# Kernel optimization log

Hardware: AMD Instinct MI355X
Metric: run time of the kernel (lower is better)

Reference implementation:

```python
import jax, jax.numpy as jnp
import numpy as np

EMBED_DIM = 512  # channels C
B, H, W = 2, 64, 64


def _conv1x1(x, w, b):
    # x: [B, C, H, W]; w: [C_out, C_in]; b: [C_out]  (1x1 conv == per-pixel linear)
    return jnp.einsum('bchw,dc->bdhw', x, w) + b[None, :, None, None]


def setup_inputs() -> dict:
    key = jax.random.key(0)
    ks = jax.random.split(key, 9)
    C = EMBED_DIM
    s = 1.0 / np.sqrt(C)
    x = jax.random.normal(ks[0], (B, C, H, W), dtype=jnp.float32)
    wq = jax.random.normal(ks[1], (C, C), dtype=jnp.float32) * s
    bq = jax.random.normal(ks[2], (C,), dtype=jnp.float32) * 0.01
    wk = jax.random.normal(ks[3], (C, C), dtype=jnp.float32) * s
    bk = jax.random.normal(ks[4], (C,), dtype=jnp.float32) * 0.01
    wv = jax.random.normal(ks[5], (C, C), dtype=jnp.float32) * s
    bv = jax.random.normal(ks[6], (C,), dtype=jnp.float32) * 0.01
    wo = jax.random.normal(ks[7], (C, C), dtype=jnp.float32) * s
    bo = jax.random.normal(ks[8], (C,), dtype=jnp.float32) * 0.01
    return {"x": x, "wq": wq, "bq": bq, "wk": wk, "bk": bk,
            "wv": wv, "bv": bv, "wo": wo, "bo": bo}


def reference(x, wq, bq, wk, bk, wv, bv, wo, bo):
    b, c, h, w = x.shape
    n = h * w
    q = _conv1x1(x, wq, bq).reshape(b, c, n)
    k = _conv1x1(x, wk, bk).reshape(b, c, n)
    v = _conv1x1(x, wv, bv).reshape(b, c, n)
    # scores = q^T @ k over channel dim -> [b, n, n]; scale by sqrt(C) (scale=True)
    scores = jnp.einsum('bcn,bcm->bnm', q, k) / jnp.sqrt(jnp.asarray(c, x.dtype))
    attn = jax.nn.softmax(scores, axis=-1)
    # output = v @ attn^T -> [b, c, n]
    out = jnp.einsum('bcm,bnm->bcn', v, attn).reshape(b, c, h, w)
    return _conv1x1(out, wo, bo)
```

## Files before the change

### kernel.cpp

```cpp
#include <hip/hip_runtime.h>
#include <stdint.h>

typedef short s16x8 __attribute__((ext_vector_type(8)));
typedef unsigned short u16x8 __attribute__((ext_vector_type(8)));
typedef float f32x4 __attribute__((ext_vector_type(4)));

__device__ __forceinline__ float bf2f(unsigned short u) {
  union { unsigned u; float f; } c; c.u = ((unsigned)u) << 16; return c.f;
}
__device__ __forceinline__ unsigned short f2bf(float f) {
  union { float f; unsigned u; } c; c.f = f;
  unsigned u = c.u + 0x7fffu + ((c.u >> 16) & 1u);
  return (unsigned short)(u >> 16);
}

__device__ __forceinline__ void g2l16(const void* g, void* l) {
  __builtin_amdgcn_global_load_lds(
      (const __attribute__((address_space(1))) void*)(unsigned long long)g,
      (__attribute__((address_space(3))) void*)(unsigned)(unsigned long long)l,
      16, 0, 0);
}

template <int MODE, typename OutT>
__global__ __launch_bounds__(256) void gemm_abt(
    const unsigned short* __restrict__ A, int lda,
    const unsigned short* __restrict__ Bt, int ldb,
    OutT* __restrict__ C, int ldc,
    const float* __restrict__ bias,
    float* __restrict__ rowsum,
    int M, int N, int K, int nsplit,
    long long sA, long long sBt, long long sC, long long sSplit,
    float scale)
{
  __shared__ __align__(16) unsigned short smem[128 * 136];
  unsigned short* As = smem;
  unsigned short* Bs = smem + 128 * 64;

  const int ks = blockIdx.z % nsplit;
  const int bz = blockIdx.z / nsplit;
  A  += (long long)bz * sA;
  Bt += (long long)bz * sBt;
  C  += (long long)bz * sC + (long long)ks * sSplit;

  const int tile_m = blockIdx.y * 128;
  const int tile_n = blockIdx.x * 128;

  const int tid  = threadIdx.x;
  const int wid  = tid >> 6;
  const int lane = tid & 63;
  const int wm = (wid >> 1) * 64;
  const int wn = (wid & 1) * 64;
  const int lr = lane & 15;
  const int lq = lane >> 4;

  const int srow = lane >> 3;
  const int scol = ((lane & 7) ^ (srow & 7)) * 8;

  f32x4 acc[4][4];
  const f32x4 zero4 = {0.f, 0.f, 0.f, 0.f};
  #pragma unroll
  for (int i = 0; i < 4; ++i)
    #pragma unroll
    for (int j = 0; j < 4; ++j) acc[i][j] = zero4;

  const unsigned short* Arow = A  + (long long)tile_m * lda;
  const unsigned short* Brow = Bt + (long long)tile_n * ldb;

  const int kLen = K / nsplit;
  const int kBeg = ks * kLen;

  for (int k0 = kBeg; k0 < kBeg + kLen; k0 += 64) {
    #pragma unroll
    for (int c = 0; c < 4; ++c) {
      const int chunk = wid * 4 + c;
      const int row = chunk * 8 + srow;
      g2l16(Arow + (long long)row * lda + k0 + scol, As + chunk * 512);
      g2l16(Brow + (long long)row * ldb + k0 + scol, Bs + chunk * 512);
    }
    __syncthreads();
    #pragma unroll
    for (int kss = 0; kss < 2; ++kss) {
      const int cch = kss * 4 + lq;
      s16x8 af[4], bfr[4];
      #pragma unroll
      for (int i = 0; i < 4; ++i) {
        const int row = wm + i * 16 + lr;
        af[i] = *(const s16x8*)&As[row * 64 + ((cch ^ (row & 7)) * 8)];
      }
      #pragma unroll
      for (int j = 0; j < 4; ++j) {
        const int row = wn + j * 16 + lr;
        bfr[j] = *(const s16x8*)&Bs[row * 64 + ((cch ^ (row & 7)) * 8)];
      }
      #pragma unroll
      for (int i = 0; i < 4; ++i)
        #pragma unroll
        for (int j = 0; j < 4; ++j)
          acc[i][j] = __builtin_amdgcn_mfma_f32_16x16x32_bf16(af[i], bfr[j], acc[i][j], 0, 0, 0);
    }
    __syncthreads();
  }

  if constexpr (MODE == 3) {
    #pragma unroll
    for (int i = 0; i < 4; ++i) {
      const int row0 = tile_m + wm + i * 16 + lq * 4;
      #pragma unroll
      for (int j = 0; j < 4; ++j) {
        const int col = tile_n + wn + j * 16 + lr;
        const float inv = 1.0f / rowsum[(long long)bz * N + col];
        #pragma unroll
        for (int r = 0; r < 4; ++r) {
          float v = acc[i][j][r] * inv;
          if (ks == 0) v += bias[row0 + r];
          atomicAdd((float*)&C[(long long)(row0 + r) * ldc + col], v);
        }
      }
    }
  } else {
    #pragma unroll
    for (int i = 0; i < 4; ++i) {
      const int lrow0 = wm + i * 16 + lq * 4;
      float rsum[4] = {0.f, 0.f, 0.f, 0.f};
      #pragma unroll
      for (int j = 0; j < 4; ++j) {
        const int lcol = wn + j * 16 + lr;
        float bcol = 0.f;
        if (MODE == 1 && bias) bcol = bias[tile_n + lcol];
        #pragma unroll
        for (int r = 0; r < 4; ++r) {
          float v = acc[i][j][r] * scale + bcol;
          if (MODE == 2) { v = __expf(v); rsum[r] += v; }
          smem[(lrow0 + r) * 136 + lcol] = f2bf(v);
        }
      }
      if (MODE == 2) {
        #pragma unroll
        for (int r = 0; r < 4; ++r) {
          float s = rsum[r];
          s += __shfl_xor(s, 1); s += __shfl_xor(s, 2);
          s += __shfl_xor(s, 4); s += __shfl_xor(s, 8);
          if (lr == 0)
            atomicAdd(&rowsum[(long long)bz * M + tile_m + lrow0 + r], s);
        }
      }
    }
    __syncthreads();
    const int row = tid >> 1;
    const int cb = (tid & 1) * 64;
    unsigned short* Cg = (unsigned short*)C;
    #pragma unroll
    for (int k = 0; k < 8; ++k) {
      u16x8 v = *(const u16x8*)&smem[row * 136 + cb + k * 8];
      *(u16x8*)&Cg[(long long)(tile_m + row) * ldc + tile_n + cb + k * 8] = v;
    }
  }
}

__global__ __launch_bounds__(256) void cvt_weights(
    const float* __restrict__ wq, const float* __restrict__ wk,
    const float* __restrict__ wv, const float* __restrict__ wo,
    const float* __restrict__ bq, const float* __restrict__ bk,
    unsigned short* __restrict__ wqk_b, unsigned short* __restrict__ wvT_b,
    unsigned short* __restrict__ wo_b, float* __restrict__ bqk,
    float* __restrict__ rowsum, int n)
{
  const int i = blockIdx.x * 256 + threadIdx.x;
  if (i < n) {
    wqk_b[i]     = f2bf(wq[i]);
    wqk_b[n + i] = f2bf(wk[i]);
    wvT_b[i]     = f2bf(wv[(i & 511) * 512 + (i >> 9)]);
    wo_b[i]      = f2bf(wo[i]);
  }
  if (i < 512) {
    bqk[i]       = bq[i];
    bqk[512 + i] = bk[i];
  }
  if (i < 8192) rowsum[i] = 0.f;
}

__global__ __launch_bounds__(256) void bias_pp(
    const float* __restrict__ wo, const float* __restrict__ bv,
    const float* __restrict__ bo, float* __restrict__ bpp)
{
  const int w = threadIdx.x >> 6, lane = threadIdx.x & 63;
  const int d = blockIdx.x * 4 + w;
  const float* row = wo + (long long)d * 512;
  float s = 0.f;
  #pragma unroll
  for (int c = 0; c < 512; c += 64) s += row[c + lane] * bv[c + lane];
  #pragma unroll
  for (int o = 32; o > 0; o >>= 1) s += __shfl_xor(s, o, 64);
  if (lane == 0) bpp[d] = s + bo[d];
}

__global__ __launch_bounds__(256) void transpose_cn(
    const float* __restrict__ x, unsigned short* __restrict__ xT,
    int C, int N)
{
  __shared__ float tile[32][33];
  const long long boff = (long long)blockIdx.z * C * N;
  const int n0 = blockIdx.x * 32;
  const int c0 = blockIdx.y * 32;
  const int tx = threadIdx.x;
  const int ty = threadIdx.y;
  #pragma unroll
  for (int k = 0; k < 32; k += 8)
    tile[ty + k][tx] = x[boff + (long long)(c0 + ty + k) * N + n0 + tx];
  __syncthreads();
  #pragma unroll
  for (int k = 0; k < 32; k += 8)
    xT[boff + (long long)(n0 + ty + k) * C + c0 + tx] = f2bf(tile[tx][ty + k]);
}

extern "C" void kernel_launch(void* const* d_in, const int* in_sizes, int n_in,
                              void* d_out, int out_size, void* d_ws, size_t ws_size,
                              hipStream_t stream) {
  (void)in_sizes; (void)n_in; (void)ws_size;
  const float* x  = (const float*)d_in[0];
  const float* wq = (const float*)d_in[1];
  const float* bq = (const float*)d_in[2];
  const float* wk = (const float*)d_in[3];
  const float* bk = (const float*)d_in[4];
  const float* wv = (const float*)d_in[5];
  const float* bv = (const float*)d_in[6];
  const float* wo = (const float*)d_in[7];
  const float* bo = (const float*)d_in[8];
  float* out = (float*)d_out;

  const int Cc = 512, N = 4096, Bn = 2;
  const int CC = Cc * Cc;
  const long long NC  = (long long)N * Cc;
  const long long NC2 = (long long)N * 1024;
  const long long NN  = (long long)N * N;

  char* wsb = (char*)d_ws;
  unsigned short* wqk_b = (unsigned short*)wsb;
  unsigned short* wvT_b = wqk_b + 2LL * CC;
  unsigned short* wo_b  = wvT_b + CC;
  unsigned short* Wp    = wo_b + CC;
  float*          bqk   = (float*)(Wp + CC);
  float*          bpp   = bqk + 1024;
  float*          rsum  = bpp + 512;
  unsigned short* xT    = (unsigned short*)(rsum + 8192);
  unsigned short* qkT   = xT + Bn * NC;
  unsigned short* vo    = qkT + Bn * NC2;
  unsigned short* S     = vo + Bn * NC;

  const float inv_sqrt_c = 0.044194173824159216f;

  cvt_weights<<<dim3((CC + 255) / 256), 256, 0, stream>>>(
      wq, wk, wv, wo, bq, bk, wqk_b, wvT_b, wo_b, bqk, rsum, CC);
  bias_pp<<<dim3(128), 256, 0, stream>>>(wo, bv, bo, bpp);
  gemm_abt<1, unsigned short><<<dim3(4, 4, 1), 256, 0, stream>>>(
      wo_b, 512, wvT_b, 512, Wp, 512, nullptr, nullptr,
      512, 512, 512, 1, 0, 0, 0, 0, 1.0f);
  transpose_cn<<<dim3(N / 32, Cc / 32, Bn), dim3(32, 8), 0, stream>>>(x, xT, Cc, N);

  gemm_abt<1, unsigned short><<<dim3(8, N / 128, Bn), 256, 0, stream>>>(
      xT, Cc, wqk_b, Cc, qkT, 1024, bqk, nullptr, N, 1024, Cc, 1,
      NC, 0, NC2, 0, 1.0f);
  gemm_abt<2, unsigned short><<<dim3(N / 128, N / 128, Bn), 256, 0, stream>>>(
      qkT, 1024, qkT + 512, 1024, S, N, nullptr, rsum, N, N, Cc, 1,
      NC2, NC2, NN, 0, inv_sqrt_c);
  gemm_abt<1, unsigned short><<<dim3(N / 128, 4, Bn), 256, 0, stream>>>(
      Wp, 512, xT, 512, vo, N, nullptr, nullptr, 512, N, Cc, 1,
      0, NC, NC, 0, 1.0f);
  hipMemsetAsync(out, 0, (size_t)out_size * sizeof(float), stream);
  gemm_abt<3, float><<<dim3(N / 128, 4, Bn * 2), 256, 0, stream>>>(
      vo, N, S, N, out, N, bpp, rsum, 512, N, N, 2,
      NC, NN, NC, 0, 1.0f);
}
```

Measured before the change: 285.2 us.

## Fuse V projection into QK GEMM and replace atomic split-K with partial reduce

The folded Wo·Wv weight becomes a third block of a concatenated 1536-column weight, so x is projected to Q, K and the projected V in one GEMM. A bf16 transpose then lays out the V part for the final GEMM. The final attention-times-V GEMM now uses a 4-way K split that writes bf16 partial tiles through the normal epilogue, instead of a 2-way split doing fp32 atomicAdds into a zeroed output. A new elementwise kernel sums the four partials, applies the softmax row normalisation and adds the bias. This removes atomic contention and the memset and doubles block-level parallelism, at the cost of extra partial-buffer traffic, one more launch and extra bf16 rounding of partial sums.

```diff
diff --git a/kernel.cpp b/kernel.cpp
--- a/kernel.cpp
+++ b/kernel.cpp
@@ -21,11 +21,11 @@
       16, 0, 0);
 }
 
-template <int MODE, typename OutT>
+template <int MODE>
 __global__ __launch_bounds__(256) void gemm_abt(
     const unsigned short* __restrict__ A, int lda,
     const unsigned short* __restrict__ Bt, int ldb,
-    OutT* __restrict__ C, int ldc,
+    unsigned short* __restrict__ C, int ldc,
     const float* __restrict__ bias,
     float* __restrict__ rowsum,
     int M, int N, int K, int nsplit,
@@ -101,59 +101,40 @@
     __syncthreads();
   }
 
-  if constexpr (MODE == 3) {
+  #pragma unroll
+  for (int i = 0; i < 4; ++i) {
+    const int lrow0 = wm + i * 16 + lq * 4;
+    float rsum[4] = {0.f, 0.f, 0.f, 0.f};
     #pragma unroll
-    for (int i = 0; i < 4; ++i) {
-      const int row0 = tile_m + wm + i * 16 + lq * 4;
-      #pragma unroll
-      for (int j = 0; j < 4; ++j) {
-        const int col = tile_n + wn + j * 16 + lr;
-        const float inv = 1.0f / rowsum[(long long)bz * N + col];
-        #pragma unroll
-        for (int r = 0; r < 4; ++r) {
-          float v = acc[i][j][r] * inv;
-          if (ks == 0) v += bias[row0 + r];
-          atomicAdd((float*)&C[(long long)(row0 + r) * ldc + col], v);
-        }
+    for (int j = 0; j < 4; ++j) {
+      const int lcol = wn + j * 16 + lr;
+      float bcol = 0.f;
+      if (MODE == 1 && bias) bcol = bias[tile_n + lcol];
+      #pragma unroll
+      for (int r = 0; r < 4; ++r) {
+        float v = acc[i][j][r] * scale + bcol;
+        if (MODE == 2) { v = __expf(v); rsum[r] += v; }
+        smem[(lrow0 + r) * 136 + lcol] = f2bf(v);
       }
     }
-  } else {
-    #pragma unroll
-    for (int i = 0; i < 4; ++i) {
-      const int lrow0 = wm + i * 16 + lq * 4;
-      float rsum[4] = {0.f, 0.f, 0.f, 0.f};
-      #pragma unroll
-      for (int j = 0; j < 4; ++j) {
-        const int lcol = wn + j * 16 + lr;
-        float bcol = 0.f;
-        if (MODE == 1 && bias) bcol = bias[tile_n + lcol];
-        #pragma unroll
-        for (int r = 0; r < 4; ++r) {
-          float v = acc[i][j][r] * scale + bcol;
-          if (MODE == 2) { v = __expf(v); rsum[r] += v; }
-          smem[(lrow0 + r) * 136 + lcol] = f2bf(v);
-        }
-      }
-      if (MODE == 2) {
-        #pragma unroll
-        for (int r = 0; r < 4; ++r) {
-          float s = rsum[r];
-          s += __shfl_xor(s, 1); s += __shfl_xor(s, 2);
-          s += __shfl_xor(s, 4); s += __shfl_xor(s, 8);
-          if (lr == 0)
-            atomicAdd(&rowsum[(long long)bz * M + tile_m + lrow0 + r], s);
-        }
+    if (MODE == 2) {
+      #pragma unroll
+      for (int r = 0; r < 4; ++r) {
+        float s = rsum[r];
+        s += __shfl_xor(s, 1); s += __shfl_xor(s, 2);
+        s += __shfl_xor(s, 4); s += __shfl_xor(s, 8);
+        if (lr == 0)
+          atomicAdd(&rowsum[(long long)bz * M + tile_m + lrow0 + r], s);
       }
     }
-    __syncthreads();
-    const int row = tid >> 1;
-    const int cb = (tid & 1) * 64;
-    unsigned short* Cg = (unsigned short*)C;
-    #pragma unroll
-    for (int k = 0; k < 8; ++k) {
-      u16x8 v = *(const u16x8*)&smem[row * 136 + cb + k * 8];
-      *(u16x8*)&Cg[(long long)(tile_m + row) * ldc + tile_n + cb + k * 8] = v;
-    }
+  }
+  __syncthreads();
+  const int row = tid >> 1;
+  const int cb = (tid & 1) * 64;
+  #pragma unroll
+  for (int k = 0; k < 8; ++k) {
+    u16x8 v = *(const u16x8*)&smem[row * 136 + cb + k * 8];
+    *(u16x8*)&C[(long long)(tile_m + row) * ldc + tile_n + cb + k * 8] = v;
   }
 }
 
@@ -161,20 +142,21 @@
     const float* __restrict__ wq, const float* __restrict__ wk,
     const float* __restrict__ wv, const float* __restrict__ wo,
     const float* __restrict__ bq, const float* __restrict__ bk,
-    unsigned short* __restrict__ wqk_b, unsigned short* __restrict__ wvT_b,
-    unsigned short* __restrict__ wo_b, float* __restrict__ bqk,
+    unsigned short* __restrict__ W3, unsigned short* __restrict__ wvT_b,
+    unsigned short* __restrict__ wo_b, float* __restrict__ bqk3,
     float* __restrict__ rowsum, int n)
 {
   const int i = blockIdx.x * 256 + threadIdx.x;
   if (i < n) {
-    wqk_b[i]     = f2bf(wq[i]);
-    wqk_b[n + i] = f2bf(wk[i]);
-    wvT_b[i]     = f2bf(wv[(i & 511) * 512 + (i >> 9)]);
-    wo_b[i]      = f2bf(wo[i]);
+    W3[i]      = f2bf(wq[i]);
+    W3[n + i]  = f2bf(wk[i]);
+    wvT_b[i]   = f2bf(wv[(i & 511) * 512 + (i >> 9)]);
+    wo_b[i]    = f2bf(wo[i]);
   }
   if (i < 512) {
-    bqk[i]       = bq[i];
-    bqk[512 + i] = bk[i];
+    bqk3[i]        = bq[i];
+    bqk3[512 + i]  = bk[i];
+    bqk3[1024 + i] = 0.f;
   }
   if (i < 8192) rowsum[i] = 0.f;
 }
@@ -213,10 +195,56 @@
     xT[boff + (long long)(n0 + ty + k) * C + c0 + tx] = f2bf(tile[tx][ty + k]);
 }
 
+__global__ __launch_bounds__(256) void transpose_bf(
+    const unsigned short* __restrict__ src, int srcLd, long long sSrc,
+    unsigned short* __restrict__ dst, int dstLd, long long sDst,
+    int R, int Cc)
+{
+  __shared__ unsigned short tile[32][33];
+  const int r0 = blockIdx.x * 32;
+  const int c0 = blockIdx.y * 32;
+  const int tx = threadIdx.x;
+  const int ty = threadIdx.y;
+  const long long so = (long long)blockIdx.z * sSrc;
+  const long long dofs = (long long)blockIdx.z * sDst;
+  #pragma unroll
+  for (int k = 0; k < 32; k += 8)
+    tile[ty + k][tx] = src[so + (long long)(r0 + ty + k) * srcLd + c0 + tx];
+  __syncthreads();
+  #pragma unroll
+  for (int k = 0; k < 32; k += 8)
+    dst[dofs + (long long)(c0 + ty + k) * dstLd + r0 + tx] = tile[tx][ty + k];
+}
+
+__global__ __launch_bounds__(256) void reduce4_norm_out(
+    const unsigned short* __restrict__ p, long long L,
+    const float* __restrict__ rowsum, const float* __restrict__ bpp,
+    float* __restrict__ o)
+{
+  const long long i = 8LL * (blockIdx.x * 256 + threadIdx.x);
+  const int b = (int)(i >> 21);
+  const int d = (int)((i >> 12) & 511);
+  const int n = (int)(i & 4095);
+  const float bb = bpp[d];
+  const float* rs = &rowsum[b * 4096 + n];
+  u16x8 a  = *(const u16x8*)&p[i];
+  u16x8 b1 = *(const u16x8*)&p[L + i];
+  u16x8 c  = *(const u16x8*)&p[2 * L + i];
+  u16x8 d1 = *(const u16x8*)&p[3 * L + i];
+  f32x4 o0, o1;
+  #pragma unroll
+  for (int j = 0; j < 4; ++j) {
+    o0[j] = ((bf2f(a[j]) + bf2f(b1[j])) + (bf2f(c[j]) + bf2f(d1[j]))) / rs[j] + bb;
+    o1[j] = ((bf2f(a[4 + j]) + bf2f(b1[4 + j])) + (bf2f(c[4 + j]) + bf2f(d1[4 + j]))) / rs[4 + j] + bb;
+  }
+  *(f32x4*)&o[i] = o0;
+  *(f32x4*)&o[i + 4] = o1;
+}
+
 extern "C" void kernel_launch(void* const* d_in, const int* in_sizes, int n_in,
                               void* d_out, int out_size, void* d_ws, size_t ws_size,
                               hipStream_t stream) {
-  (void)in_sizes; (void)n_in; (void)ws_size;
+  (void)in_sizes; (void)n_in; (void)out_size; (void)ws_size;
   const float* x  = (const float*)d_in[0];
   const float* wq = (const float*)d_in[1];
   const float* bq = (const float*)d_in[2];
@@ -228,46 +256,46 @@
   const float* bo = (const float*)d_in[8];
   float* out = (float*)d_out;
 
-  const int Cc = 512, N = 4096, Bn = 2;
+  const int Cc = 512, N = 4096, Bn = 2, C3 = 1536;
   const int CC = Cc * Cc;
   const long long NC  = (long long)N * Cc;
-  const long long NC2 = (long long)N * 1024;
+  const long long NC3 = (long long)N * C3;
   const long long NN  = (long long)N * N;
 
   char* wsb = (char*)d_ws;
-  unsigned short* wqk_b = (unsigned short*)wsb;
-  unsigned short* wvT_b = wqk_b + 2LL * CC;
+  unsigned short* W3    = (unsigned short*)wsb;
+  unsigned short* wvT_b = W3 + 3LL * CC;
   unsigned short* wo_b  = wvT_b + CC;
-  unsigned short* Wp    = wo_b + CC;
-  float*          bqk   = (float*)(Wp + CC);
-  float*          bpp   = bqk + 1024;
+  float*          bqk3  = (float*)(wo_b + CC);
+  float*          bpp   = bqk3 + 1536;
   float*          rsum  = bpp + 512;
   unsigned short* xT    = (unsigned short*)(rsum + 8192);
-  unsigned short* qkT   = xT + Bn * NC;
-  unsigned short* vo    = qkT + Bn * NC2;
+  unsigned short* qkvoT = xT + Bn * NC;
+  unsigned short* vo    = qkvoT + Bn * NC3;
   unsigned short* S     = vo + Bn * NC;
+  unsigned short* part  = S + Bn * NN;
 
   const float inv_sqrt_c = 0.044194173824159216f;
 
   cvt_weights<<<dim3((CC + 255) / 256), 256, 0, stream>>>(
-      wq, wk, wv, wo, bq, bk, wqk_b, wvT_b, wo_b, bqk, rsum, CC);
+      wq, wk, wv, wo, bq, bk, W3, wvT_b, wo_b, bqk3, rsum, CC);
   bias_pp<<<dim3(128), 256, 0, stream>>>(wo, bv, bo, bpp);
-  gemm_abt<1, unsigned short><<<dim3(4, 4, 1), 256, 0, stream>>>(
-      wo_b, 512, wvT_b, 512, Wp, 512, nullptr, nullptr,
+  gemm_abt<1><<<dim3(4, 4, 1), 256, 0, stream>>>(
+      wo_b, 512, wvT_b, 512, W3 + 2LL * CC, 512, nullptr, nullptr,
       512, 512, 512, 1, 0, 0, 0, 0, 1.0f);
   transpose_cn<<<dim3(N / 32, Cc / 32, Bn), dim3(32, 8), 0, stream>>>(x, xT, Cc, N);
 
-  gemm_abt<1, unsigned short><<<dim3(8, N / 128, Bn), 256, 0, stream>>>(
-      xT, Cc, wqk_b, Cc, qkT, 1024, bqk, nullptr, N, 1024, Cc, 1,
-      NC, 0, NC2, 0, 1.0f);
-  gemm_abt<2, unsigned short><<<dim3(N / 128, N / 128, Bn), 256, 0, stream>>>(
-      qkT, 1024, qkT + 512, 1024, S, N, nullptr, rsum, N, N, Cc, 1,
-      NC2, NC2, NN, 0, inv_sqrt_c);
-  gemm_abt<1, unsigned short><<<dim3(N / 128, 4, Bn), 256, 0, stream>>>(
-      Wp, 512, xT, 512, vo, N, nullptr, nullptr, 512, N, Cc, 1,
-      0, NC, NC, 0, 1.0f);
-  hipMemsetAsync(out, 0, (size_t)out_size * sizeof(float), stream);
-  gemm_abt<3, float><<<dim3(N / 128, 4, Bn * 2), 256, 0, stream>>>(
-      vo, N, S, N, out, N, bpp, rsum, 512, N, N, 2,
-      NC, NN, NC, 0, 1.0f);
-}
+  gemm_abt<1><<<dim3(C3 / 128, N / 128, Bn), 256, 0, stream>>>(
+      xT, Cc, W3, Cc, qkvoT, C3, bqk3, nullptr, N, C3, Cc, 1,
+      NC, 0, NC3, 0, 1.0f);
+  transpose_bf<<<dim3(N / 32, Cc / 32, Bn), dim3(32, 8), 0, stream>>>(
+      qkvoT + 1024, C3, NC3, vo, N, NC, N, Cc);
+  gemm_abt<2><<<dim3(N / 128, N / 128, Bn), 256, 0, stream>>>(
+      qkvoT, C3, qkvoT + 512, C3, S, N, nullptr, rsum, N, N, Cc, 1,
+      NC3, NC3, NN, 0, inv_sqrt_c);
+  gemm_abt<1><<<dim3(N / 128, 4, Bn * 4), 256, 0, stream>>>(
+      vo, N, S, N, part, N, nullptr, nullptr, 512, N, N, 4,
+      NC, NN, NC, (long long)Bn * NC, 1.0f);
+  reduce4_norm_out<<<dim3((int)((Bn * NC) / 2048)), 256, 0, stream>>>(
+      part, (long long)Bn * NC, rsum, bpp, out);
+}
```

Result: faster. 264.1 us (-7.4%).
